# Performance work log

Hardware: AMD Instinct MI355X
Metric: run time of the kernel (lower is better)

## Reference

```python
import jax, jax.numpy as jnp
import numpy as np

SEQ, H, NC = 20, 128, 100000

def _lstm_cell(x, h, c, Wih, Whh, bih, bhh):
    # gates: [B, 4H] in PyTorch order i, f, g, o
    g = x @ Wih.T + bih + h @ Whh.T + bhh
    i, f, gg, o = jnp.split(g, 4, axis=-1)
    c2 = jax.nn.sigmoid(f) * c + jax.nn.sigmoid(i) * jnp.tanh(gg)
    h2 = jax.nn.sigmoid(o) * jnp.tanh(c2)
    return h2, c2

def setup_inputs() -> dict:
    key = jax.random.key(0)
    ks = jax.random.split(key, 24)
    u = lambda k, shp, bound: jax.random.uniform(k, shp, jnp.float32, -bound, bound)
    s1 = 1.0 / np.sqrt(H)       # PyTorch LSTMCell init bound, hidden_size=H
    s2 = 1.0 / np.sqrt(2 * H)   # combined cell, hidden_size=2H
    kn = lambda k, shp: jax.random.normal(k, shp, jnp.float32) * np.sqrt(2.0 / shp[1])  # kaiming_normal_
    return {
        'x': jax.random.normal(ks[0], (SEQ, 1, H), jnp.float32),
        'h0f': kn(ks[1], (1, H)), 'c0f': kn(ks[2], (1, H)),
        'h0b': kn(ks[3], (1, H)), 'c0b': kn(ks[4], (1, H)),
        'h0l': kn(ks[5], (1, 2 * H)), 'c0l': kn(ks[6], (1, 2 * H)),
        'Wih_f': u(ks[7], (4 * H, H), s1), 'Whh_f': u(ks[8], (4 * H, H), s1),
        'bih_f': u(ks[9], (4 * H,), s1), 'bhh_f': u(ks[10], (4 * H,), s1),
        'Wih_b': u(ks[11], (4 * H, H), s1), 'Whh_b': u(ks[12], (4 * H, H), s1),
        'bih_b': u(ks[13], (4 * H,), s1), 'bhh_b': u(ks[14], (4 * H,), s1),
        'Wih_l': u(ks[15], (8 * H, 2 * H), s2), 'Whh_l': u(ks[16], (8 * H, 2 * H), s2),
        'bih_l': u(ks[17], (8 * H,), s2), 'bhh_l': u(ks[18], (8 * H,), s2),
        'Wlin': u(ks[19], (NC, 2 * H), 1.0 / np.sqrt(2 * H)),
        'blin': u(ks[20], (NC,), 1.0 / np.sqrt(2 * H)),
    }

def reference(x, h0f, c0f, h0b, c0b, h0l, c0l,
              Wih_f, Whh_f, bih_f, bhh_f,
              Wih_b, Whh_b, bih_b, bhh_b,
              Wih_l, Whh_l, bih_l, bhh_l,
              Wlin, blin):
    xs = x.reshape(SEQ, 1, H)

    def step_f(carry, xt):
        h, c = _lstm_cell(xt, carry[0], carry[1], Wih_f, Whh_f, bih_f, bhh_f)
        return (h, c), h
    _, fwd = jax.lax.scan(step_f, (h0f, c0f), xs)          # [SEQ, 1, H]

    def step_b(carry, xt):
        h, c = _lstm_cell(xt, carry[0], carry[1], Wih_b, Whh_b, bih_b, bhh_b)
        return (h, c), h
    # backward list is kept in reversed-scan order (NOT flipped back), per source zip
    _, bwd = jax.lax.scan(step_b, (h0b, c0b), xs[::-1])    # [SEQ, 1, H]

    comb = jnp.concatenate([fwd, bwd], axis=-1)            # [SEQ, 1, 2H]

    def step_l(carry, xt):
        h, c = _lstm_cell(xt, carry[0], carry[1], Wih_l, Whh_l, bih_l, bhh_l)
        return (h, c), h
    _, hl = jax.lax.scan(step_l, (h0l, c0l), comb)         # [SEQ, 1, 2H]

    fb = hl.reshape(SEQ, 2 * H)
    return fb @ Wlin.T + blin                              # [SEQ, NC]
```

## Files before the change

kernel.cpp:

```cpp
#include <hip/hip_runtime.h>
#include <stdint.h>

#define SEQ  20
#define H1   128
#define H2   256
#define NCLS 100000

#define AQ  __ATOMIC_ACQUIRE
#define RL  __ATOMIC_RELEASE
#define RX  __ATOMIC_RELAXED
#define AG  __HIP_MEMORY_SCOPE_AGENT

#define KEEPF4(v) asm volatile("" : "+v"((v).x), "+v"((v).y), "+v"((v).z), "+v"((v).w))

__device__ __forceinline__ float sigm(float x) { return 1.0f / (1.0f + __expf(-x)); }
__device__ __forceinline__ float tanhfast(float x) {
    float e = __expf(-2.0f * fabsf(x));
    float t = (1.0f - e) / (1.0f + e);
    return copysignf(t, x);
}

__global__ __launch_bounds__(1024, 1) void k_l1(
    const float* __restrict__ x,
    const float* __restrict__ h0f, const float* __restrict__ c0f,
    const float* __restrict__ h0b, const float* __restrict__ c0b,
    const float* __restrict__ WihF, const float* __restrict__ WhhF,
    const float* __restrict__ bihF, const float* __restrict__ bhhF,
    const float* __restrict__ WihB, const float* __restrict__ WhhB,
    const float* __restrict__ bihB, const float* __restrict__ bhhB,
    float* __restrict__ comb)
{
    const int dir = blockIdx.x;
    const float* Wih = dir ? WihB : WihF;
    const float* Whh = dir ? WhhB : WhhF;
    const float* bih = dir ? bihB : bihF;
    const float* bhh = dir ? bhhB : bhhF;
    const float* h0  = dir ? h0b  : h0f;
    const float* c0  = dir ? c0b  : c0f;

    __shared__ __align__(16) float smem[16032];
    float* xs      = smem;
    float* hcur    = xs + 2560;
    float* biasL   = hcur + 128;
    float* gxs     = biasL + 512;
    float* partial = gxs + 10752;

    const int tid = threadIdx.x;

    for (int i = tid; i < SEQ * H1; i += 1024) xs[i] = x[i];
    if (tid < 4 * H1) biasL[tid] = bih[tid] + bhh[tid];
    if (tid < H1) hcur[tid] = h0[tid];
    float cregA = 0.f, cregB = 0.f;
    if (tid < 64) { cregA = c0[tid]; cregB = c0[tid + 64]; }

    const int pr = tid >> 1, ph = tid & 1;
    {
        float4 wf[16];
        const float4* p = (const float4*)(Wih + pr * H1 + ph * 64);
#pragma unroll
        for (int j = 0; j < 16; ++j) { wf[j] = p[j]; KEEPF4(wf[j]); }
        __syncthreads();
        for (int t = 0; t < SEQ; ++t) {
            const int tx = dir ? (SEQ - 1 - t) : t;
            const float4* xp = (const float4*)(xs + tx * H1 + ph * 64);
            float a = 0.f;
#pragma unroll
            for (int j = 0; j < 16; ++j) {
                float4 v = xp[j];
                a += wf[j].x * v.x + wf[j].y * v.y + wf[j].z * v.z + wf[j].w * v.w;
            }
            a += __shfl_xor(a, 1);
            if (ph == 0) gxs[pr * 21 + t] = a + biasL[pr];
        }
    }

    const int cg = tid >> 8, r0 = (tid & 255) * 2;
    float4 wa[8], wb[8];
    {
        const float4* pa = (const float4*)(Whh + r0 * H1 + cg * 32);
        const float4* pb = (const float4*)(Whh + (r0 + 1) * H1 + cg * 32);
#pragma unroll
        for (int j = 0; j < 8; ++j) {
            wa[j] = pa[j]; KEEPF4(wa[j]);
            wb[j] = pb[j]; KEEPF4(wb[j]);
        }
    }
    __syncthreads();

    for (int t = 0; t < SEQ; ++t) {
        const float4* hp = (const float4*)(hcur + cg * 32);
        float a0 = 0.f, a1 = 0.f;
#pragma unroll
        for (int j = 0; j < 8; ++j) {
            float4 v = hp[j];
            a0 += wa[j].x * v.x + wa[j].y * v.y + wa[j].z * v.z + wa[j].w * v.w;
            a1 += wb[j].x * v.x + wb[j].y * v.y + wb[j].z * v.z + wb[j].w * v.w;
        }
        *(float2*)(partial + cg * 520 + r0) = make_float2(a0, a1);
        __syncthreads();
        if (tid < 64) {
            const int c = tid;
            float s0[4], s1[4];
#pragma unroll
            for (int g = 0; g < 4; ++g) {
                float accA = gxs[(g * H1 + c) * 21 + t];
                float accB = gxs[(g * H1 + c + 64) * 21 + t];
#pragma unroll
                for (int q = 0; q < 4; ++q) {
                    accA += partial[q * 520 + g * H1 + c];
                    accB += partial[q * 520 + g * H1 + c + 64];
                }
                s0[g] = accA; s1[g] = accB;
            }
            float cnA = sigm(s0[1]) * cregA + sigm(s0[0]) * tanhfast(s0[2]);
            float cnB = sigm(s1[1]) * cregB + sigm(s1[0]) * tanhfast(s1[2]);
            cregA = cnA; cregB = cnB;
            float hA = sigm(s0[3]) * tanhfast(cnA);
            float hB = sigm(s1[3]) * tanhfast(cnB);
            hcur[c] = hA; hcur[c + 64] = hB;
            comb[t * H2 + dir * H1 + c]      = hA;
            comb[t * H2 + dir * H1 + c + 64] = hB;
        }
        __syncthreads();
    }
}

__global__ __launch_bounds__(1024, 1) void k_l2(
    const float* __restrict__ Whhl,
    const float* __restrict__ h0l, const float* __restrict__ c0l,
    const float* __restrict__ Wihl,
    const float* __restrict__ bihl, const float* __restrict__ bhhl,
    const float* __restrict__ comb,
    float* __restrict__ fb,
    float* __restrict__ hg2,
    int* __restrict__ flags)
{
    const int bid = blockIdx.x;
    if (bid & 7) return;
    const int s   = bid >> 3;
    const int tid = threadIdx.x;

    __shared__ __align__(16) float smem[12048];
    float* cs      = smem;
    float* hc2     = cs + 5120;
    float* bias2   = hc2 + 256;
    float* partial = bias2 + 256;
    float* gxs     = partial + 1040;

    const int cg = tid >> 8;
    const int L  = tid & 255;
    const int R  = (L >> 6) * H2 + s * 64 + (L & 63);

    for (int i = tid; i < SEQ * H2; i += 1024) cs[i] = comb[i];
    if (tid < 256) { bias2[tid] = bihl[R] + bhhl[R]; hc2[tid] = h0l[tid]; }
    float creg = (tid < 64) ? c0l[s * 64 + tid] : 0.0f;

    float4 w[16];
    {
        const float4* p = (const float4*)(Wihl + (size_t)R * H2 + cg * 64);
#pragma unroll
        for (int j = 0; j < 16; ++j) { w[j] = p[j]; KEEPF4(w[j]); }
    }
    __syncthreads();
    for (int t = 0; t < SEQ; ++t) {
        const float4* cp = (const float4*)(cs + t * H2 + cg * 64);
        float a = 0.f;
#pragma unroll
        for (int j = 0; j < 16; ++j) {
            float4 v = cp[j];
            a += w[j].x * v.x + w[j].y * v.y + w[j].z * v.z + w[j].w * v.w;
        }
        partial[cg * 260 + L] = a;
        __syncthreads();
        if (tid < 256)
            gxs[tid * 21 + t] = bias2[tid] + partial[tid] + partial[260 + tid]
                              + partial[520 + tid] + partial[780 + tid];
        __syncthreads();
    }

    {
        const float4* p = (const float4*)(Whhl + (size_t)R * H2 + cg * 64);
#pragma unroll
        for (int j = 0; j < 16; ++j) { w[j] = p[j]; KEEPF4(w[j]); }
    }
    __syncthreads();

    for (int t = 0; t < SEQ; ++t) {
        const float4* hp = (const float4*)(hc2 + cg * 64);
        float a = 0.f;
#pragma unroll
        for (int j = 0; j < 16; ++j) {
            float4 v = hp[j];
            a += w[j].x * v.x + w[j].y * v.y + w[j].z * v.z + w[j].w * v.w;
        }
        partial[cg * 260 + L] = a;
        __syncthreads();
        if (tid < 64) {
            const int c = tid;
            float sg[4];
#pragma unroll
            for (int g = 0; g < 4; ++g) {
                float acc = gxs[(g * 64 + c) * 21 + t];
#pragma unroll
                for (int q = 0; q < 4; ++q)
                    acc += partial[q * 260 + g * 64 + c];
                sg[g] = acc;
            }
            float cn = sigm(sg[1]) * creg + sigm(sg[0]) * tanhfast(sg[2]);
            creg = cn;
            float hn = sigm(sg[3]) * tanhfast(cn);
            fb[t * H2 + s * 64 + c] = hn;
            hc2[s * 64 + c] = hn;
            if (t + 1 < SEQ) {
                __hip_atomic_store(&hg2[(t & 1) * H2 + s * 64 + c], hn, RX, AG);
                if (tid == 0)
                    __hip_atomic_store(&flags[s * 32], t + 1, RL, AG);
            }
        } else if (tid >= 64 && tid < 112 && t + 1 < SEQ) {
            const int l  = tid - 64;
            const int rs = (s + 1 + (l >> 4)) & 3;
            const int base = rs * 64 + (l & 15) * 4;
            while (__hip_atomic_load(&flags[rs * 32], AQ, AG) < t + 1)
                __builtin_amdgcn_s_sleep(1);
#pragma unroll
            for (int j = 0; j < 4; ++j)
                hc2[base + j] =
                    __hip_atomic_load(&hg2[(t & 1) * H2 + base + j], RX, AG);
        }
        __syncthreads();
    }
}

__global__ __launch_bounds__(256, 4) void k_out4(
    const float* __restrict__ Wlin, const float* __restrict__ blin,
    const float* __restrict__ fb, float* __restrict__ out)
{
    __shared__ __align__(16) float fbs[H2 * SEQ];
    __shared__ float obuf[64 * 21];
    const int tid = threadIdx.x;
    for (int t = 0; t < SEQ; ++t) fbs[tid * SEQ + t] = fb[t * H2 + tid];
    __syncthreads();

    const int base = blockIdx.x * 64;
    const int c = tid >> 2, q = tid & 3;
    const int n = base + c;

    float acc[SEQ];
#pragma unroll
    for (int t = 0; t < SEQ; ++t) acc[t] = 0.f;

    if (n < NCLS) {
        const float* wp = Wlin + (size_t)n * H2 + q * 64;
        const float* fp = fbs + (q * 64) * SEQ;
        for (int k = 0; k < 64; k += 4) {
            float4 wv = *(const float4*)(wp + k);
            const float* f0 = fp + k * SEQ;
#pragma unroll
            for (int t = 0; t < SEQ; t += 4) {
                float4 a0 = *(const float4*)(f0 + t);
                float4 a1 = *(const float4*)(f0 + SEQ + t);
                float4 a2 = *(const float4*)(f0 + 2 * SEQ + t);
                float4 a3 = *(const float4*)(f0 + 3 * SEQ + t);
                acc[t]     += wv.x * a0.x + wv.y * a1.x + wv.z * a2.x + wv.w * a3.x;
                acc[t + 1] += wv.x * a0.y + wv.y * a1.y + wv.z * a2.y + wv.w * a3.y;
                acc[t + 2] += wv.x * a0.z + wv.y * a1.z + wv.z * a2.z + wv.w * a3.z;
                acc[t + 3] += wv.x * a0.w + wv.y * a1.w + wv.z * a2.w + wv.w * a3.w;
            }
        }
    }
#pragma unroll
    for (int t = 0; t < SEQ; ++t) {
        acc[t] += __shfl_xor(acc[t], 1);
        acc[t] += __shfl_xor(acc[t], 2);
    }
    if (q == 0) {
#pragma unroll
        for (int t = 0; t < SEQ; ++t) obuf[c * 21 + t] = acc[t];
    }
    __syncthreads();
    for (int i = tid; i < 64 * SEQ; i += 256) {
        const int t = i >> 6, cc = i & 63;
        const int n2 = base + cc;
        if (n2 < NCLS)
            out[(size_t)t * NCLS + n2] = obuf[cc * 21 + t] + blin[n2];
    }
}

extern "C" void kernel_launch(void* const* d_in, const int* in_sizes, int n_in,
                              void* d_out, int out_size, void* d_ws, size_t ws_size,
                              hipStream_t stream)
{
    const float* x    = (const float*)d_in[0];
    const float* h0f_ = (const float*)d_in[1];
    const float* c0f_ = (const float*)d_in[2];
    const float* h0b_ = (const float*)d_in[3];
    const float* c0b_ = (const float*)d_in[4];
    const float* h0l_ = (const float*)d_in[5];
    const float* c0l_ = (const float*)d_in[6];
    const float* WihF = (const float*)d_in[7];
    const float* WhhF = (const float*)d_in[8];
    const float* bihF = (const float*)d_in[9];
    const float* bhhF = (const float*)d_in[10];
    const float* WihB = (const float*)d_in[11];
    const float* WhhB = (const float*)d_in[12];
    const float* bihB = (const float*)d_in[13];
    const float* bhhB = (const float*)d_in[14];
    const float* Wihl = (const float*)d_in[15];
    const float* Whhl = (const float*)d_in[16];
    const float* bihl = (const float*)d_in[17];
    const float* bhhl = (const float*)d_in[18];
    const float* Wlin = (const float*)d_in[19];
    const float* blin = (const float*)d_in[20];

    char* ws = (char*)d_ws;
    int*   flags = (int*)ws;
    float* hg2   = (float*)(ws + 2048);
    float* comb  = (float*)(ws + 4096);
    float* fb    = (float*)(ws + 24576);

    hipMemsetAsync(flags, 0, 2048, stream);

    k_l1<<<2, 1024, 0, stream>>>(x, h0f_, c0f_, h0b_, c0b_,
                                 WihF, WhhF, bihF, bhhF,
                                 WihB, WhhB, bihB, bhhB, comb);
    k_l2<<<32, 1024, 0, stream>>>(Whhl, h0l_, c0l_,
                                  Wihl, bihl, bhhl,
                                  comb, fb, hg2, flags);
    k_out4<<<(NCLS + 63) / 64, 256, 0, stream>>>(Wlin, blin, fb, (float*)d_out);
}
```

Before: 389.6 us.

## Remap output GEMV threads by K-quarter and prefetch weight rows into registers

The output projection kernel now assigns each wavefront a quarter of the K dimension for 64 classes, instead of four adjacent lanes per class. Each thread loads its 64 weights into registers before the shared-memory barrier, so global loads overlap the fb staging. Partial sums are reduced through shared memory rather than lane shuffles, and q==0 threads write outputs directly. The aim is more memory-level parallelism on the 100 MB weight stream. In exchange, weight loads now stride 1 KB across lanes and are less coalesced, and register pressure rises with 64 weight floats plus 20 accumulators per thread.

```diff
diff --git a/kernel.cpp b/kernel.cpp
--- a/kernel.cpp
+++ b/kernel.cpp
@@ -231,30 +231,37 @@
     }
 }
 
-__global__ __launch_bounds__(256, 4) void k_out4(
+__global__ __launch_bounds__(256, 4) void k_out_w(
     const float* __restrict__ Wlin, const float* __restrict__ blin,
     const float* __restrict__ fb, float* __restrict__ out)
 {
     __shared__ __align__(16) float fbs[H2 * SEQ];
-    __shared__ float obuf[64 * 21];
+    __shared__ float part[3 * 64 * 21];
     const int tid = threadIdx.x;
+    const int q   = tid >> 6;
+    const int c   = tid & 63;
+    const int n   = blockIdx.x * 64 + c;
+
     for (int t = 0; t < SEQ; ++t) fbs[tid * SEQ + t] = fb[t * H2 + tid];
-    __syncthreads();
-
-    const int base = blockIdx.x * 64;
-    const int c = tid >> 2, q = tid & 3;
-    const int n = base + c;
+
+    float4 wreg[16];
+    if (n < NCLS) {
+        const float4* wp = (const float4*)(Wlin + (size_t)n * H2 + q * 64);
+#pragma unroll
+        for (int j = 0; j < 16; ++j) wreg[j] = wp[j];
+    }
+    __syncthreads();
 
     float acc[SEQ];
 #pragma unroll
     for (int t = 0; t < SEQ; ++t) acc[t] = 0.f;
 
     if (n < NCLS) {
-        const float* wp = Wlin + (size_t)n * H2 + q * 64;
         const float* fp = fbs + (q * 64) * SEQ;
-        for (int k = 0; k < 64; k += 4) {
-            float4 wv = *(const float4*)(wp + k);
-            const float* f0 = fp + k * SEQ;
+#pragma unroll
+        for (int j = 0; j < 16; ++j) {
+            float4 wv = wreg[j];
+            const float* f0 = fp + (j * 4) * SEQ;
 #pragma unroll
             for (int t = 0; t < SEQ; t += 4) {
                 float4 a0 = *(const float4*)(f0 + t);
@@ -268,21 +275,23 @@
             }
         }
     }
-#pragma unroll
-    for (int t = 0; t < SEQ; ++t) {
-        acc[t] += __shfl_xor(acc[t], 1);
-        acc[t] += __shfl_xor(acc[t], 2);
-    }
-    if (q == 0) {
-#pragma unroll
-        for (int t = 0; t < SEQ; ++t) obuf[c * 21 + t] = acc[t];
-    }
-    __syncthreads();
-    for (int i = tid; i < 64 * SEQ; i += 256) {
-        const int t = i >> 6, cc = i & 63;
-        const int n2 = base + cc;
-        if (n2 < NCLS)
-            out[(size_t)t * NCLS + n2] = obuf[cc * 21 + t] + blin[n2];
+
+    if (q > 0) {
+        float* pp = part + ((q - 1) * 64 + c) * 21;
+#pragma unroll
+        for (int t = 0; t < SEQ; ++t) pp[t] = acc[t];
+    }
+    __syncthreads();
+    if (q == 0 && n < NCLS) {
+        const float* p0 = part + c * 21;
+        const float* p1 = part + (64 + c) * 21;
+        const float* p2 = part + (128 + c) * 21;
+        float bv = blin[n];
+#pragma unroll
+        for (int t = 0; t < SEQ; ++t) {
+            float v = acc[t] + p0[t] + p1[t] + p2[t] + bv;
+            out[(size_t)t * NCLS + n] = v;
+        }
     }
 }
 
@@ -326,5 +335,5 @@
     k_l2<<<32, 1024, 0, stream>>>(Whhl, h0l_, c0l_,
                                   Wihl, bihl, bhhl,
                                   comb, fb, hg2, flags);
-    k_out4<<<(NCLS + 63) / 64, 256, 0, stream>>>(Wlin, blin, fb, (float*)d_out);
-}
+    k_out_w<<<(NCLS + 63) / 64, 256, 0, stream>>>(Wlin, blin, fb, (float*)d_out);
+}
```

Result: slower. 485.7 us (+24.7%).
